# Optimization experiments

Measured on AMD Instinct MI355X. Metric: run time of the kernel, lower is better.

Reference implementation:

```python
import jax, jax.numpy as jnp
import numpy as np
from jax import lax

DN = ('NCHW', 'OIHW', 'NCHW')
EPS_BN = 1e-5
EPS_NORM = 1e-8
THRESH = 0.5


def _conv(x, w, b, p):
    y = lax.conv_general_dilated(x, w, (1, 1), [(p, p), (p, p)], dimension_numbers=DN)
    return y + b[None, :, None, None]


def _bn(x, g, be, m, v):
    # inference-mode BatchNorm2d using running stats
    inv = g * lax.rsqrt(v + EPS_BN)
    return x * inv[None, :, None, None] + (be - m * inv)[None, :, None, None]


def _lrelu(x):
    return jnp.where(x >= 0, x, 0.01 * x)


def _cnn(x, p):
    # Convlayer: residual conv stack, 1 -> 16 -> 32 -> 32 -> 1 channels
    residual = x
    x = _lrelu(_bn(_conv(x, p['w1'], p['b1'], 1), p['g1'], p['be1'], p['m1'], p['v1']))
    x = _lrelu(_bn(_conv(x, p['w2'], p['b2'], 1), p['g2'], p['be2'], p['m2'], p['v2']))
    x = _lrelu(_bn(_conv(x, p['w3'], p['b3'], 2), p['g3'], p['be3'], p['m3'], p['v3']))
    x = _bn(_conv(x, p['w4'], p['b4'], 1), p['g4'], p['be4'], p['m4'], p['v4'])
    return _lrelu(x + residual)


def _make_params(key):
    ks = jax.random.split(key, 32)
    ki = iter(ks)
    def w(shape, fan_in):
        return jax.random.normal(next(ki), shape, jnp.float32) * (1.0 / np.sqrt(fan_in))
    def bn(c):
        return (1.0 + 0.1 * jax.random.normal(next(ki), (c,), jnp.float32),
                0.1 * jax.random.normal(next(ki), (c,), jnp.float32),
                0.1 * jax.random.normal(next(ki), (c,), jnp.float32),
                0.5 + jax.random.uniform(next(ki), (c,), jnp.float32))
    p = {}
    p['w0'] = w((1, 3, 3, 3), 27); p['b0'] = jnp.zeros((1,), jnp.float32)
    p['w1'] = w((16, 1, 3, 3), 9); p['b1'] = jnp.zeros((16,), jnp.float32)
    p['g1'], p['be1'], p['m1'], p['v1'] = bn(16)
    p['w2'] = w((32, 16, 3, 3), 144); p['b2'] = jnp.zeros((32,), jnp.float32)
    p['g2'], p['be2'], p['m2'], p['v2'] = bn(32)
    p['w3'] = w((32, 32, 5, 5), 800); p['b3'] = jnp.zeros((32,), jnp.float32)
    p['g3'], p['be3'], p['m3'], p['v3'] = bn(32)
    p['w4'] = w((1, 32, 3, 3), 288); p['b4'] = jnp.zeros((1,), jnp.float32)
    p['g4'], p['be4'], p['m4'], p['v4'] = bn(1)
    return p


def setup_inputs() -> dict:
    key = jax.random.key(0)
    k_gt, k_refs, k_p = jax.random.split(key, 3)
    B, R, H, W = 8, 4, 256, 256
    inp = {
        'gt': jax.random.normal(k_gt, (B, 3, H, W), jnp.float32),
        'refs': jax.random.normal(k_refs, (B, R, 1, H, W), jnp.float32),
    }
    inp.update(_make_params(k_p))
    return inp


def reference(gt, refs,
              w0, b0,
              w1, b1, g1, be1, m1, v1,
              w2, b2, g2, be2, m2, v2,
              w3, b3, g3, be3, m3, v3,
              w4, b4, g4, be4, m4, v4):
    p = dict(w1=w1, b1=b1, g1=g1, be1=be1, m1=m1, v1=v1,
             w2=w2, b2=b2, g2=g2, be2=be2, m2=m2, v2=v2,
             w3=w3, b3=b3, g3=g3, be3=be3, m3=m3, v3=v3,
             w4=w4, b4=b4, g4=g4, be4=be4, m4=m4, v4=v4)
    B, R, _, H, W = refs.shape
    gt1 = _conv(gt, w0, b0, 1)                 # [B,1,H,W]
    gt_feat = _cnn(gt1, p)                     # [B,1,H,W]
    refs_feat = _cnn(refs.reshape(B * R, 1, H, W), p).reshape(B, R, 1, H, W)
    diff_maps = jnp.abs(gt_feat[:, None] - refs_feat)          # [B,R,1,H,W]
    total = diff_maps.sum(axis=2)                              # [B,R,H,W]
    mn = total.min(axis=1, keepdims=True)
    mx = total.max(axis=1, keepdims=True)
    norm = jnp.clip((total - mn) / (mx - mn + EPS_NORM), 0.1, 1.0)
    dissim_map = jnp.where(norm > THRESH, norm, jnp.zeros_like(norm))  # [B,R,H,W]
    ref_idx = jnp.argmax(dissim_map, axis=1)[:, None]          # [B,1,H,W]
    # collage loop == gather of refs_feat along the ref axis
    collage = jnp.take_along_axis(refs_feat[:, :, 0], ref_idx, axis=1)  # [B,1,H,W]
    return dissim_map, collage
```

## Files before the change

kernel.cpp:

```cpp
#include <hip/hip_runtime.h>
#include <math.h>

#define HW 256
#define NPIX 65536

__device__ __forceinline__ float lrelu(float x) { return x >= 0.f ? x : 0.01f * x; }

__global__ __launch_bounds__(256) void conv0_kernel(const float* __restrict__ gt,
                                                    const float* __restrict__ w0,
                                                    const float* __restrict__ b0,
                                                    float* __restrict__ gt1) {
  int idx = blockIdx.x * 256 + threadIdx.x;
  int n = idx >> 16;
  int px = idx & 65535;
  int y = px >> 8, x = px & 255;
  float acc = b0[0];
  #pragma unroll
  for (int c = 0; c < 3; ++c) {
    const float* src = gt + (size_t)(n * 3 + c) * NPIX;
    #pragma unroll
    for (int ky = 0; ky < 3; ++ky) {
      int yy = y + ky - 1;
      if (yy < 0 || yy > 255) continue;
      #pragma unroll
      for (int kx = 0; kx < 3; ++kx) {
        int xx = x + kx - 1;
        if (xx < 0 || xx > 255) continue;
        acc = fmaf(src[yy * HW + xx], w0[(c * 3 + ky) * 3 + kx], acc);
      }
    }
  }
  gt1[idx] = acc;
}

__global__ __launch_bounds__(256) void conv1_kernel(const float* __restrict__ gt1,
                                                    const float* __restrict__ refs,
                                                    const float* __restrict__ w1,
                                                    const float* __restrict__ b1,
                                                    const float* __restrict__ g1,
                                                    const float* __restrict__ be1,
                                                    const float* __restrict__ m1,
                                                    const float* __restrict__ v1,
                                                    float* __restrict__ out, int i0) {
  __shared__ float sIn[34 * 34];
  __shared__ float sW[144];
  __shared__ float sScale[16], sShift[16];
  const int t = threadIdx.x;
  const int nz = blockIdx.z, n = i0 + nz;
  const int X0 = blockIdx.x * 32, Y0 = blockIdx.y * 32;
  const float* src = (n < 8) ? (gt1 + (size_t)n * NPIX) : (refs + (size_t)(n - 8) * NPIX);
  for (int id = t; id < 34 * 34; id += 256) {
    int row = id / 34, col = id - row * 34;
    int gy = Y0 + row - 1, gx = X0 + col - 1;
    float val = 0.f;
    if (gy >= 0 && gy < HW && gx >= 0 && gx < HW) val = src[gy * HW + gx];
    sIn[id] = val;
  }
  if (t < 144) sW[t] = w1[t];
  if (t < 16) {
    float inv = g1[t] / sqrtf(v1[t] + 1e-5f);
    sScale[t] = inv;
    sShift[t] = b1[t] * inv + be1[t] - m1[t] * inv;
  }
  __syncthreads();
  const int tx = t & 15, ty = t >> 4;
  const int lx = tx * 2, ly = ty * 2;
  float rin[4][4];
  #pragma unroll
  for (int r = 0; r < 4; ++r)
    #pragma unroll
    for (int c = 0; c < 4; ++c) rin[r][c] = sIn[(ly + r) * 34 + lx + c];
  #pragma unroll
  for (int oc = 0; oc < 16; ++oc) {
    float wv[9];
    #pragma unroll
    for (int k = 0; k < 9; ++k) wv[k] = sW[oc * 9 + k];
    float a[2][2] = {{0.f, 0.f}, {0.f, 0.f}};
    #pragma unroll
    for (int ky = 0; ky < 3; ++ky)
      #pragma unroll
      for (int kx = 0; kx < 3; ++kx) {
        const float wc = wv[ky * 3 + kx];
        a[0][0] = fmaf(rin[ky][kx], wc, a[0][0]);
        a[0][1] = fmaf(rin[ky][kx + 1], wc, a[0][1]);
        a[1][0] = fmaf(rin[ky + 1][kx], wc, a[1][0]);
        a[1][1] = fmaf(rin[ky + 1][kx + 1], wc, a[1][1]);
      }
    const float sc = sScale[oc], sh = sShift[oc];
    #pragma unroll
    for (int dy = 0; dy < 2; ++dy)
      #pragma unroll
      for (int dx = 0; dx < 2; ++dx) {
        int gy = Y0 + ly + dy, gx = X0 + lx + dx;
        out[(size_t)(nz * 16 + oc) * NPIX + gy * HW + gx] = lrelu(a[dy][dx] * sc + sh);
      }
  }
}

template <int CIN, int K>
__global__ __launch_bounds__(256, 2) void convT2_kernel(const float* __restrict__ in,
                                                        const float* __restrict__ w,
                                                        const float* __restrict__ bias,
                                                        const float* __restrict__ gg,
                                                        const float* __restrict__ be,
                                                        const float* __restrict__ mm,
                                                        const float* __restrict__ vv_,
                                                        float* __restrict__ out) {
  constexpr int KK = K * K;
  constexpr int PAD = K / 2;
  constexpr int ROWS = 16 + K - 1;
  constexpr int NIN = ROWS * 36;
  constexpr int RR = 2 + K - 1;
  __shared__ float sIn[NIN];
  __shared__ float sScale[32], sShift[32];
  const int t = threadIdx.x;
  if (t < 32) {
    float inv = gg[t] / sqrtf(vv_[t] + 1e-5f);
    sScale[t] = inv;
    sShift[t] = bias[t] * inv + be[t] - mm[t] * inv;
  }
  const int X0 = blockIdx.x * 32, Y0 = blockIdx.y * 16;
  const int nz = blockIdx.z;
  const int wave = __builtin_amdgcn_readfirstlane(t >> 6);
  const int lane = t & 63;
  const int lx = lane & 7, ly = lane >> 3;
  const int x0l = lx * 4, y0l = ly * 2;
  const int oc0 = wave * 8;
  const float* inN = in + (size_t)nz * CIN * NPIX;
  const float* wb = w + (size_t)oc0 * CIN * KK;

  int soff[3];
  bool svalid[3];
  #pragma unroll
  for (int q = 0; q < 3; ++q) {
    int id = t + q * 256;
    int row = id / 36, col = id - row * 36;
    int gy = Y0 + row - PAD, gx = X0 + col - PAD;
    svalid[q] = (id < NIN) && gy >= 0 && gy < HW && gx >= 0 && gx < HW && (col < 32 + 2 * PAD);
    soff[q] = gy * HW + gx;
  }

  float acc[8][2][4];
  #pragma unroll
  for (int j = 0; j < 8; ++j)
    #pragma unroll
    for (int py = 0; py < 2; ++py)
      #pragma unroll
      for (int px = 0; px < 4; ++px) acc[j][py][px] = 0.f;

  float vi[3];
  #pragma unroll
  for (int q = 0; q < 3; ++q) vi[q] = svalid[q] ? inN[soff[q]] : 0.f;

  for (int ic = 0; ic < CIN; ++ic) {
    #pragma unroll
    for (int q = 0; q < 3; ++q) {
      int id = t + q * 256;
      if (id < NIN) sIn[id] = vi[q];
    }
    __syncthreads();
    if (ic + 1 < CIN) {
      const float* src = inN + (size_t)(ic + 1) * NPIX;
      #pragma unroll
      for (int q = 0; q < 3; ++q) vi[q] = svalid[q] ? src[soff[q]] : 0.f;
    }
    float rin[RR][8];
    #pragma unroll
    for (int r = 0; r < RR; ++r) {
      const float4 a4 = *reinterpret_cast<const float4*>(&sIn[(y0l + r) * 36 + x0l]);
      const float4 b4 = *reinterpret_cast<const float4*>(&sIn[(y0l + r) * 36 + x0l + 4]);
      rin[r][0] = a4.x; rin[r][1] = a4.y; rin[r][2] = a4.z; rin[r][3] = a4.w;
      rin[r][4] = b4.x; rin[r][5] = b4.y; rin[r][6] = b4.z; rin[r][7] = b4.w;
    }
    #pragma unroll
    for (int j = 0; j < 8; ++j) {
      const float* wp = wb + ((size_t)j * CIN + ic) * KK;
      float wr[KK];
      #pragma unroll
      for (int k = 0; k < KK; ++k) wr[k] = wp[k];
      #pragma unroll
      for (int ky = 0; ky < K; ++ky)
        #pragma unroll
        for (int kx = 0; kx < K; ++kx) {
          const float wc = wr[ky * K + kx];
          #pragma unroll
          for (int py = 0; py < 2; ++py)
            #pragma unroll
            for (int px = 0; px < 4; ++px)
              acc[j][py][px] = fmaf(rin[py + ky][px + kx], wc, acc[j][py][px]);
        }
    }
    __syncthreads();
  }

  float* outN = out + (size_t)nz * 32 * NPIX;
  #pragma unroll
  for (int j = 0; j < 8; ++j) {
    const float sc = sScale[oc0 + j], sh = sShift[oc0 + j];
    #pragma unroll
    for (int py = 0; py < 2; ++py) {
      float4 o;
      o.x = lrelu(acc[j][py][0] * sc + sh);
      o.y = lrelu(acc[j][py][1] * sc + sh);
      o.z = lrelu(acc[j][py][2] * sc + sh);
      o.w = lrelu(acc[j][py][3] * sc + sh);
      *reinterpret_cast<float4*>(
          &outN[(size_t)(oc0 + j) * NPIX + (Y0 + y0l + py) * HW + X0 + x0l]) = o;
    }
  }
}

__global__ __launch_bounds__(256) void conv4_kernel(const float* __restrict__ in,
                                                    const float* __restrict__ gt1,
                                                    const float* __restrict__ refs,
                                                    const float* __restrict__ w4,
                                                    const float* __restrict__ b4,
                                                    const float* __restrict__ g4,
                                                    const float* __restrict__ be4,
                                                    const float* __restrict__ m4,
                                                    const float* __restrict__ v4,
                                                    float* __restrict__ feat, int i0) {
  __shared__ float sIn[34 * 34];
  const int t = threadIdx.x;
  const int nz = blockIdx.z, n = i0 + nz;
  const int X0 = blockIdx.x * 32, Y0 = blockIdx.y * 32;
  const int tx = t & 15, ty = t >> 4;
  const int lx = tx * 2, ly = ty * 2;
  const float* inN = in + (size_t)nz * 32 * NPIX;

  int soff[5];
  bool svalid[5];
  #pragma unroll
  for (int q = 0; q < 5; ++q) {
    int id = t + q * 256;
    int row = id / 34, col = id - row * 34;
    int gy = Y0 + row - 1, gx = X0 + col - 1;
    svalid[q] = (id < 34 * 34) && gy >= 0 && gy < HW && gx >= 0 && gx < HW;
    soff[q] = gy * HW + gx;
  }

  float a[2][2] = {{0.f, 0.f}, {0.f, 0.f}};
  float vi[5];
  #pragma unroll
  for (int q = 0; q < 5; ++q) vi[q] = svalid[q] ? inN[soff[q]] : 0.f;

  for (int ic = 0; ic < 32; ++ic) {
    #pragma unroll
    for (int q = 0; q < 5; ++q) {
      int id = t + q * 256;
      if (id < 34 * 34) sIn[id] = vi[q];
    }
    __syncthreads();
    if (ic + 1 < 32) {
      const float* src = inN + (size_t)(ic + 1) * NPIX;
      #pragma unroll
      for (int q = 0; q < 5; ++q) vi[q] = svalid[q] ? src[soff[q]] : 0.f;
    }
    float rin[4][4];
    #pragma unroll
    for (int r = 0; r < 4; ++r) {
      const float2 p0 = *reinterpret_cast<const float2*>(&sIn[(ly + r) * 34 + lx]);
      const float2 p1 = *reinterpret_cast<const float2*>(&sIn[(ly + r) * 34 + lx + 2]);
      rin[r][0] = p0.x; rin[r][1] = p0.y; rin[r][2] = p1.x; rin[r][3] = p1.y;
    }
    const float* wp = w4 + ic * 9;
    float wv[9];
    #pragma unroll
    for (int k = 0; k < 9; ++k) wv[k] = wp[k];
    #pragma unroll
    for (int ky = 0; ky < 3; ++ky)
      #pragma unroll
      for (int kx = 0; kx < 3; ++kx) {
        const float wc = wv[ky * 3 + kx];
        a[0][0] = fmaf(rin[ky][kx], wc, a[0][0]);
        a[0][1] = fmaf(rin[ky][kx + 1], wc, a[0][1]);
        a[1][0] = fmaf(rin[ky + 1][kx], wc, a[1][0]);
        a[1][1] = fmaf(rin[ky + 1][kx + 1], wc, a[1][1]);
      }
    __syncthreads();
  }
  const float inv = g4[0] / sqrtf(v4[0] + 1e-5f);
  const float sh = b4[0] * inv + be4[0] - m4[0] * inv;
  const float* res = (n < 8) ? (gt1 + (size_t)n * NPIX) : (refs + (size_t)(n - 8) * NPIX);
  #pragma unroll
  for (int dy = 0; dy < 2; ++dy)
    #pragma unroll
    for (int dx = 0; dx < 2; ++dx) {
      int px = (Y0 + ly + dy) * HW + X0 + lx + dx;
      float val = a[dy][dx] * inv + sh + res[px];
      feat[(size_t)n * NPIX + px] = lrelu(val);
    }
}

__global__ __launch_bounds__(256) void final_kernel(const float* __restrict__ feat,
                                                    float* __restrict__ outD) {
  int idx = blockIdx.x * 256 + threadIdx.x;
  int b = idx >> 16, px = idx & 65535;
  float gv = feat[(size_t)b * NPIX + px];
  float tv[4];
  float mn = 1e30f, mx = -1e30f;
  #pragma unroll
  for (int r = 0; r < 4; ++r) {
    float rv = feat[(size_t)(8 + b * 4 + r) * NPIX + px];
    tv[r] = fabsf(gv - rv);
    mn = fminf(mn, tv[r]);
    mx = fmaxf(mx, tv[r]);
  }
  const float denom = mx - mn + 1e-8f;
  float d[4];
  #pragma unroll
  for (int r = 0; r < 4; ++r) {
    float nrm = (tv[r] - mn) / denom;
    nrm = fminf(fmaxf(nrm, 0.1f), 1.0f);
    d[r] = nrm > 0.5f ? nrm : 0.f;
    outD[(size_t)(b * 4 + r) * NPIX + px] = d[r];
  }
  int best = 0;
  float bv = d[0];
  #pragma unroll
  for (int r = 1; r < 4; ++r)
    if (d[r] > bv) { bv = d[r]; best = r; }
  outD[(size_t)32 * NPIX + (size_t)b * NPIX + px] =
      feat[(size_t)(8 + b * 4 + best) * NPIX + px];
}

extern "C" void kernel_launch(void* const* d_in, const int* in_sizes, int n_in,
                              void* d_out, int out_size, void* d_ws, size_t ws_size,
                              hipStream_t stream) {
  const float* gt   = (const float*)d_in[0];
  const float* refs = (const float*)d_in[1];
  const float* w0 = (const float*)d_in[2];
  const float* b0 = (const float*)d_in[3];
  const float* w1 = (const float*)d_in[4];
  const float* b1 = (const float*)d_in[5];
  const float* g1 = (const float*)d_in[6];
  const float* be1 = (const float*)d_in[7];
  const float* m1 = (const float*)d_in[8];
  const float* v1 = (const float*)d_in[9];
  const float* w2 = (const float*)d_in[10];
  const float* b2 = (const float*)d_in[11];
  const float* g2 = (const float*)d_in[12];
  const float* be2 = (const float*)d_in[13];
  const float* m2 = (const float*)d_in[14];
  const float* v2 = (const float*)d_in[15];
  const float* w3 = (const float*)d_in[16];
  const float* b3 = (const float*)d_in[17];
  const float* g3 = (const float*)d_in[18];
  const float* be3 = (const float*)d_in[19];
  const float* m3 = (const float*)d_in[20];
  const float* v3 = (const float*)d_in[21];
  const float* w4 = (const float*)d_in[22];
  const float* b4 = (const float*)d_in[23];
  const float* g4 = (const float*)d_in[24];
  const float* be4 = (const float*)d_in[25];
  const float* m4 = (const float*)d_in[26];
  const float* v4 = (const float*)d_in[27];

  float* ws = (float*)d_ws;
  float* gt1  = ws;
  float* feat = gt1 + (size_t)8 * NPIX;
  float* bufBase = feat + (size_t)40 * NPIX;

  size_t fixedBytes = (size_t)(8 + 40) * NPIX * sizeof(float);
  size_t avail = (ws_size > fixedBytes) ? (ws_size - fixedBytes) : 0;
  size_t perImg = (size_t)2 * 32 * NPIX * sizeof(float);
  int maxC = (int)(avail / perImg);
  static const int divs[8] = {40, 20, 10, 8, 5, 4, 2, 1};
  int chunk = 1;
  for (int i = 0; i < 8; ++i)
    if (divs[i] <= maxC) { chunk = divs[i]; break; }

  float* bufA = bufBase;
  float* bufB = bufA + (size_t)chunk * 32 * NPIX;

  conv0_kernel<<<2048, 256, 0, stream>>>(gt, w0, b0, gt1);

  for (int i0 = 0; i0 < 40; i0 += chunk) {
    conv1_kernel<<<dim3(8, 8, chunk), 256, 0, stream>>>(gt1, refs, w1, b1, g1, be1, m1, v1,
                                                        bufA, i0);
    convT2_kernel<16, 3><<<dim3(8, 16, chunk), 256, 0, stream>>>(bufA, w2, b2, g2, be2, m2, v2,
                                                                 bufB);
    convT2_kernel<32, 5><<<dim3(8, 16, chunk), 256, 0, stream>>>(bufB, w3, b3, g3, be3, m3, v3,
                                                                 bufA);
    conv4_kernel<<<dim3(8, 8, chunk), 256, 0, stream>>>(bufA, gt1, refs, w4, b4, g4, be4, m4,
                                                        v4, feat, i0);
  }

  final_kernel<<<2048, 256, 0, stream>>>(feat, (float*)d_out);
}
```

Baseline: 1.937 ms.

## Double-buffer shared input tiles and split output channels across 512-thread blocks

The tiled conv kernels now use double-buffered shared memory, so the next channel's tile is written while the current one is being computed. This removes one of the two barriers per input channel. The 3x3 and 5x5 conv blocks grow to 512 threads with 4 output channels per wave instead of 8, which lowers per-thread accumulator pressure and raises parallelism. Weights for the next output channel are prefetched into registers. In exchange, each block uses twice as much LDS, and with launch bounds of (512,2) register limits may cap occupancy; per-channel input tiles are also loaded by more waves for fewer outputs each.

```diff
diff --git a/kernel.cpp b/kernel.cpp
--- a/kernel.cpp
+++ b/kernel.cpp
@@ -98,7 +98,7 @@
 }
 
 template <int CIN, int K>
-__global__ __launch_bounds__(256, 2) void convT2_kernel(const float* __restrict__ in,
+__global__ __launch_bounds__(512, 2) void convT3_kernel(const float* __restrict__ in,
                                                         const float* __restrict__ w,
                                                         const float* __restrict__ bias,
                                                         const float* __restrict__ gg,
@@ -110,8 +110,9 @@
   constexpr int PAD = K / 2;
   constexpr int ROWS = 16 + K - 1;
   constexpr int NIN = ROWS * 36;
+  constexpr int NQ = (NIN + 511) / 512;
   constexpr int RR = 2 + K - 1;
-  __shared__ float sIn[NIN];
+  __shared__ float sIn[2][NIN];
   __shared__ float sScale[32], sShift[32];
   const int t = threadIdx.x;
   if (t < 32) {
@@ -123,79 +124,102 @@
   const int nz = blockIdx.z;
   const int wave = __builtin_amdgcn_readfirstlane(t >> 6);
   const int lane = t & 63;
-  const int lx = lane & 7, ly = lane >> 3;
-  const int x0l = lx * 4, y0l = ly * 2;
-  const int oc0 = wave * 8;
+  const int x0l = (lane & 7) * 4, y0l = (lane >> 3) * 2;
+  const int oc0 = wave * 4;
   const float* inN = in + (size_t)nz * CIN * NPIX;
   const float* wb = w + (size_t)oc0 * CIN * KK;
 
-  int soff[3];
-  bool svalid[3];
-  #pragma unroll
-  for (int q = 0; q < 3; ++q) {
-    int id = t + q * 256;
+  int soff[NQ];
+  bool svalid[NQ];
+  #pragma unroll
+  for (int q = 0; q < NQ; ++q) {
+    int id = t + q * 512;
     int row = id / 36, col = id - row * 36;
     int gy = Y0 + row - PAD, gx = X0 + col - PAD;
     svalid[q] = (id < NIN) && gy >= 0 && gy < HW && gx >= 0 && gx < HW && (col < 32 + 2 * PAD);
     soff[q] = gy * HW + gx;
   }
 
-  float acc[8][2][4];
-  #pragma unroll
-  for (int j = 0; j < 8; ++j)
+  float acc[4][2][4];
+  #pragma unroll
+  for (int j = 0; j < 4; ++j)
     #pragma unroll
     for (int py = 0; py < 2; ++py)
       #pragma unroll
       for (int px = 0; px < 4; ++px) acc[j][py][px] = 0.f;
 
-  float vi[3];
-  #pragma unroll
-  for (int q = 0; q < 3; ++q) vi[q] = svalid[q] ? inN[soff[q]] : 0.f;
-
+  float vi[NQ];
+  #pragma unroll
+  for (int q = 0; q < NQ; ++q) vi[q] = svalid[q] ? inN[soff[q]] : 0.f;
+  #pragma unroll
+  for (int q = 0; q < NQ; ++q) {
+    int id = t + q * 512;
+    if (id < NIN) sIn[0][id] = vi[q];
+  }
+  #pragma unroll
+  for (int q = 0; q < NQ; ++q) vi[q] = svalid[q] ? inN[NPIX + soff[q]] : 0.f;
+  __syncthreads();
+
+  int cur = 0;
   for (int ic = 0; ic < CIN; ++ic) {
-    #pragma unroll
-    for (int q = 0; q < 3; ++q) {
-      int id = t + q * 256;
-      if (id < NIN) sIn[id] = vi[q];
-    }
-    __syncthreads();
-    if (ic + 1 < CIN) {
-      const float* src = inN + (size_t)(ic + 1) * NPIX;
-      #pragma unroll
-      for (int q = 0; q < 3; ++q) vi[q] = svalid[q] ? src[soff[q]] : 0.f;
-    }
+    const float* sBase = sIn[cur];
     float rin[RR][8];
     #pragma unroll
     for (int r = 0; r < RR; ++r) {
-      const float4 a4 = *reinterpret_cast<const float4*>(&sIn[(y0l + r) * 36 + x0l]);
-      const float4 b4 = *reinterpret_cast<const float4*>(&sIn[(y0l + r) * 36 + x0l + 4]);
+      const float4 a4 = *reinterpret_cast<const float4*>(&sBase[(y0l + r) * 36 + x0l]);
+      const float4 b4 = *reinterpret_cast<const float4*>(&sBase[(y0l + r) * 36 + x0l + 4]);
       rin[r][0] = a4.x; rin[r][1] = a4.y; rin[r][2] = a4.z; rin[r][3] = a4.w;
       rin[r][4] = b4.x; rin[r][5] = b4.y; rin[r][6] = b4.z; rin[r][7] = b4.w;
     }
-    #pragma unroll
-    for (int j = 0; j < 8; ++j) {
-      const float* wp = wb + ((size_t)j * CIN + ic) * KK;
-      float wr[KK];
-      #pragma unroll
-      for (int k = 0; k < KK; ++k) wr[k] = wp[k];
+    if (ic + 1 < CIN) {
+      float* sNxt = sIn[cur ^ 1];
+      #pragma unroll
+      for (int q = 0; q < NQ; ++q) {
+        int id = t + q * 512;
+        if (id < NIN) sNxt[id] = vi[q];
+      }
+    }
+    if (ic + 2 < CIN) {
+      const float* src = inN + (size_t)(ic + 2) * NPIX;
+      #pragma unroll
+      for (int q = 0; q < NQ; ++q) vi[q] = svalid[q] ? src[soff[q]] : 0.f;
+    }
+    float wcur[KK], wnxt[KK];
+    {
+      const float* wp = wb + (size_t)ic * KK;
+      #pragma unroll
+      for (int k = 0; k < KK; ++k) wcur[k] = wp[k];
+    }
+    #pragma unroll
+    for (int j = 0; j < 4; ++j) {
+      if (j < 3) {
+        const float* wp = wb + ((size_t)(j + 1) * CIN + ic) * KK;
+        #pragma unroll
+        for (int k = 0; k < KK; ++k) wnxt[k] = wp[k];
+      }
       #pragma unroll
       for (int ky = 0; ky < K; ++ky)
         #pragma unroll
         for (int kx = 0; kx < K; ++kx) {
-          const float wc = wr[ky * K + kx];
+          const float wc = wcur[ky * K + kx];
           #pragma unroll
           for (int py = 0; py < 2; ++py)
             #pragma unroll
             for (int px = 0; px < 4; ++px)
               acc[j][py][px] = fmaf(rin[py + ky][px + kx], wc, acc[j][py][px]);
         }
+      if (j < 3) {
+        #pragma unroll
+        for (int k = 0; k < KK; ++k) wcur[k] = wnxt[k];
+      }
     }
     __syncthreads();
+    cur ^= 1;
   }
 
   float* outN = out + (size_t)nz * 32 * NPIX;
   #pragma unroll
-  for (int j = 0; j < 8; ++j) {
+  for (int j = 0; j < 4; ++j) {
     const float sc = sScale[oc0 + j], sh = sShift[oc0 + j];
     #pragma unroll
     for (int py = 0; py < 2; ++py) {
@@ -220,7 +244,7 @@
                                                     const float* __restrict__ m4,
                                                     const float* __restrict__ v4,
                                                     float* __restrict__ feat, int i0) {
-  __shared__ float sIn[34 * 34];
+  __shared__ float sIn[2][34 * 34];
   const int t = threadIdx.x;
   const int nz = blockIdx.z, n = i0 + nz;
   const int X0 = blockIdx.x * 32, Y0 = blockIdx.y * 32;
@@ -243,25 +267,37 @@
   float vi[5];
   #pragma unroll
   for (int q = 0; q < 5; ++q) vi[q] = svalid[q] ? inN[soff[q]] : 0.f;
-
+  #pragma unroll
+  for (int q = 0; q < 5; ++q) {
+    int id = t + q * 256;
+    if (id < 34 * 34) sIn[0][id] = vi[q];
+  }
+  #pragma unroll
+  for (int q = 0; q < 5; ++q) vi[q] = svalid[q] ? inN[NPIX + soff[q]] : 0.f;
+  __syncthreads();
+
+  int cur = 0;
   for (int ic = 0; ic < 32; ++ic) {
-    #pragma unroll
-    for (int q = 0; q < 5; ++q) {
-      int id = t + q * 256;
-      if (id < 34 * 34) sIn[id] = vi[q];
-    }
-    __syncthreads();
+    const float* sBase = sIn[cur];
+    float rin[4][4];
+    #pragma unroll
+    for (int r = 0; r < 4; ++r) {
+      const float2 p0 = *reinterpret_cast<const float2*>(&sBase[(ly + r) * 34 + lx]);
+      const float2 p1 = *reinterpret_cast<const float2*>(&sBase[(ly + r) * 34 + lx + 2]);
+      rin[r][0] = p0.x; rin[r][1] = p0.y; rin[r][2] = p1.x; rin[r][3] = p1.y;
+    }
     if (ic + 1 < 32) {
-      const float* src = inN + (size_t)(ic + 1) * NPIX;
+      float* sNxt = sIn[cur ^ 1];
+      #pragma unroll
+      for (int q = 0; q < 5; ++q) {
+        int id = t + q * 256;
+        if (id < 34 * 34) sNxt[id] = vi[q];
+      }
+    }
+    if (ic + 2 < 32) {
+      const float* src = inN + (size_t)(ic + 2) * NPIX;
       #pragma unroll
       for (int q = 0; q < 5; ++q) vi[q] = svalid[q] ? src[soff[q]] : 0.f;
-    }
-    float rin[4][4];
-    #pragma unroll
-    for (int r = 0; r < 4; ++r) {
-      const float2 p0 = *reinterpret_cast<const float2*>(&sIn[(ly + r) * 34 + lx]);
-      const float2 p1 = *reinterpret_cast<const float2*>(&sIn[(ly + r) * 34 + lx + 2]);
-      rin[r][0] = p0.x; rin[r][1] = p0.y; rin[r][2] = p1.x; rin[r][3] = p1.y;
     }
     const float* wp = w4 + ic * 9;
     float wv[9];
@@ -278,6 +314,7 @@
         a[1][1] = fmaf(rin[ky + 1][kx + 1], wc, a[1][1]);
       }
     __syncthreads();
+    cur ^= 1;
   }
   const float inv = g4[0] / sqrtf(v4[0] + 1e-5f);
   const float sh = b4[0] * inv + be4[0] - m4[0] * inv;
@@ -378,9 +415,9 @@
   for (int i0 = 0; i0 < 40; i0 += chunk) {
     conv1_kernel<<<dim3(8, 8, chunk), 256, 0, stream>>>(gt1, refs, w1, b1, g1, be1, m1, v1,
                                                         bufA, i0);
-    convT2_kernel<16, 3><<<dim3(8, 16, chunk), 256, 0, stream>>>(bufA, w2, b2, g2, be2, m2, v2,
+    convT3_kernel<16, 3><<<dim3(8, 16, chunk), 512, 0, stream>>>(bufA, w2, b2, g2, be2, m2, v2,
                                                                  bufB);
-    convT2_kernel<32, 5><<<dim3(8, 16, chunk), 256, 0, stream>>>(bufB, w3, b3, g3, be3, m3, v3,
+    convT3_kernel<32, 5><<<dim3(8, 16, chunk), 512, 0, stream>>>(bufB, w3, b3, g3, be3, m3, v3,
                                                                  bufA);
     conv4_kernel<<<dim3(8, 8, chunk), 256, 0, stream>>>(bufA, gt1, refs, w4, b4, g4, be4, m4,
                                                         v4, feat, i0);
```

Result: slower. 2.765 ms (+42.8%).
